# Kernel tuning notes

Hardware: AMD Instinct MI355X
Metric: run time of the kernel (lower is better)

Reference implementation:

```python
import jax, jax.numpy as jnp
import numpy as np


def setup_inputs() -> dict:
    key = jax.random.key(0)
    k1, k2, k3 = jax.random.split(key, 3)
    B, N, L, K, H = 8, 256, 32, 3, 64
    X = jax.random.normal(k1, (B, N, N, L), dtype=jnp.float32)
    G = jax.random.uniform(k2, (K, N, N), dtype=jnp.float32)
    W = jax.random.normal(k3, (K * K * L, H), dtype=jnp.float32) * (2.0 / (K * K * L + H)) ** 0.5
    b = jnp.zeros((H,), dtype=jnp.float32)
    return {"X": X, "G": G, "W": W, "b": b}


def reference(X, G, W, b):
    # X: [b, n, c, l], G: [K, N, N] diffusion supports (n == c == N)
    # Stage 1: diffuse along origin-node axis for all K supports at once.
    m1 = jnp.einsum('bncl,knm->kbmcl', X, G)            # [K, b, m, c, l]
    # Stage 2: diffuse along destination-node axis; lay out so flattening
    # (k, j, l) reproduces torch.cat order (o outer, d inner, feature last).
    m2 = jnp.einsum('kbmcl,jcd->bmdkjl', m1, G)         # [b, m, d, K, K, l]
    B, M, D = m2.shape[0], m2.shape[1], m2.shape[2]
    feat = m2.reshape(B, M, D, -1)                      # [b, m, d, K^2 * l]
    H = jnp.einsum('bmdk,kh->bmdh', feat, W) + b        # [b, m, d, hidden]
    return jax.nn.relu(H)
```

## Files before the change

### kernel.cpp

```cpp
#include <hip/hip_runtime.h>
#include <hip/hip_bf16.h>

#define NB 8
#define NN 256
#define NL 32
#define NQ 8192
#define NH 64
#define SL ((size_t)NQ * NN)

typedef __attribute__((ext_vector_type(8))) short short8v;
typedef __attribute__((ext_vector_type(4))) float float4v;
typedef __attribute__((ext_vector_type(16))) float float16v;

static __device__ __forceinline__ ushort f2bf(float f) {
  __hip_bfloat16 h = __float2bfloat16(f);
  return *reinterpret_cast<const ushort*>(&h);
}
static __device__ __forceinline__ uint packbf(float a, float b) {
  return (uint)f2bf(a) | ((uint)f2bf(b) << 16);
}
static __device__ __forceinline__ void gld_lds16(const void* g, void* l) {
  __builtin_amdgcn_global_load_lds(
      (const __attribute__((address_space(1))) unsigned int*)g,
      (__attribute__((address_space(3))) unsigned int*)l, 16, 0, 0);
}

__global__ __launch_bounds__(256) void prep_g(const float* __restrict__ G,
                                              ushort* __restrict__ Gt) {
  __shared__ float t[32][33];
  const int k = blockIdx.z, m0 = blockIdx.x * 32, n0 = blockIdx.y * 32;
  const int tid = threadIdx.x;
  const int c = tid & 31, r8 = tid >> 5;
#pragma unroll
  for (int i = 0; i < 4; ++i) {
    int r = r8 + i * 8;
    t[r][c] = G[((size_t)k * NN + n0 + r) * NN + m0 + c];
  }
  __syncthreads();
#pragma unroll
  for (int i = 0; i < 4; ++i) {
    int rm = r8 + i * 8;
    Gt[((size_t)k * NN + m0 + rm) * NN + n0 + c] = f2bf(t[c][rm]);
  }
}

__global__ __launch_bounds__(256) void prep_wf(const float* __restrict__ W,
                                               ushort* __restrict__ WtF) {
  const int tid = threadIdx.x;
  for (int e = tid; e < 9 * 2 * 2 * 64; e += 256) {
    const int ln = e & 63, hb = (e >> 6) & 1, kp = (e >> 7) & 1, kj = e >> 8;
    const int h = hb * 32 + (ln & 31);
    const int c0 = kj * 32 + kp * 16 + (ln >> 5) * 8;
    ushort v[8];
#pragma unroll
    for (int i = 0; i < 8; ++i) v[i] = f2bf(W[(size_t)(c0 + i) * NH + h]);
    *(ulong2*)(WtF + (size_t)e * 8) = *(ulong2*)v;
  }
}

__global__ __launch_bounds__(256) void prep_x(const float* __restrict__ X,
                                              ushort* __restrict__ Xt) {
  __shared__ float t[32][33];
  const int qt = blockIdx.x;
  const int n0 = blockIdx.y * 32;
  const int b  = blockIdx.z;
  const int tid = threadIdx.x;
  const int c = tid & 31, r8 = tid >> 5;
  const float* Xb = X + (size_t)b * NN * NQ;
  ushort* Xo = Xt + (size_t)b * SL;
  const size_t q0 = (size_t)qt * 32;
#pragma unroll
  for (int i = 0; i < 4; ++i) {
    int r = r8 + i * 8;
    t[r][c] = Xb[(size_t)(n0 + r) * NQ + q0 + c];
  }
  __syncthreads();
#pragma unroll
  for (int i = 0; i < 4; ++i) {
    int l = r8 + i * 8;
    Xo[((size_t)l * NN + qt) * NN + n0 + c] = f2bf(t[c][l]);
  }
}

__global__ __launch_bounds__(256) void gemm_bt(
    const ushort* __restrict__ A, const ushort* __restrict__ Bt,
    ushort* __restrict__ C, int N, int K,
    size_t aMs, size_t bDs, size_t cs) {
  __shared__ short As[128][40];
  __shared__ short Bs[128][40];
  const int z = blockIdx.z;
  A  += (size_t)(z % 3) * aMs;
  Bt += (size_t)(z / 3) * bDs;
  C  += (size_t)z * cs;
  const int n0 = blockIdx.x * 128;
  const int m0 = blockIdx.y * 128;
  const int tid = threadIdx.x;
  const int lane = tid & 63;
  const int w = tid >> 6;
  const int wr = (w >> 1) * 64, wc = (w & 1) * 64;
  const int sr = tid >> 1, sc = (tid & 1) * 16;
  const int fr = lane & 15, fg = (lane >> 4) * 8;

  float4v acc[4][4] = {};

  const ushort* ap = A + (size_t)(m0 + sr) * K + sc;
  const ushort* bp = Bt + (size_t)(n0 + sr) * K + sc;

  for (int kk = 0; kk < K; kk += 32) {
    *(float4*)&As[sr][sc]     = *(const float4*)(ap + kk);
    *(float4*)&As[sr][sc + 8] = *(const float4*)(ap + kk + 8);
    *(float4*)&Bs[sr][sc]     = *(const float4*)(bp + kk);
    *(float4*)&Bs[sr][sc + 8] = *(const float4*)(bp + kk + 8);
    __syncthreads();
    short8v af[4], bf[4];
#pragma unroll
    for (int i = 0; i < 4; ++i)
      af[i] = *(const short8v*)&As[wr + i * 16 + fr][fg];
#pragma unroll
    for (int j = 0; j < 4; ++j)
      bf[j] = *(const short8v*)&Bs[wc + j * 16 + fr][fg];
#pragma unroll
    for (int i = 0; i < 4; ++i)
#pragma unroll
      for (int j = 0; j < 4; ++j)
        acc[i][j] = __builtin_amdgcn_mfma_f32_16x16x32_bf16(af[i], bf[j],
                                                            acc[i][j], 0, 0, 0);
    __syncthreads();
  }

  const int rbase = (lane >> 4) * 4;
#pragma unroll
  for (int i = 0; i < 4; ++i) {
    const int row = m0 + wr + i * 16 + rbase;
#pragma unroll
    for (int j = 0; j < 4; ++j) {
      const int col = n0 + wc + j * 16 + fr;
      ushort* cp = C + (size_t)row * N + col;
#pragma unroll
      for (int r = 0; r < 4; ++r)
        cp[(size_t)r * N] = f2bf(acc[i][j][r]);
    }
  }
}

__global__ __launch_bounds__(256, 2) void fused_s23(
    const ushort* __restrict__ T1, const ushort* __restrict__ Gt,
    const ushort* __restrict__ WtF, const float* __restrict__ bias,
    float* __restrict__ out) {
  __shared__ ulong2 LDSQ[4096];
  char* base = (char*)LDSQ;

  const int tid = threadIdx.x;
  const int f = blockIdx.x;
  const int lid = (f & 7) * 128 + (f >> 3);
  const int dblk = lid & 1;
  const int mp   = (lid >> 1) & 63;
  const int b    = lid >> 7;

  const int lane = tid & 63;
  const int w  = tid >> 6;
  const int l5 = lane & 31;
  const int h5 = lane >> 5;
  const int wml = (w >> 1) * 64;
  const int wd  = (w & 1) * 64;
  const int d0  = dblk * 128;

  const ushort* t1b  = T1 + ((size_t)b * 3) * SL + (size_t)mp * 128 * 256;
  const ushort* gtb0 = Gt + (size_t)d0 * NN;

  auto stage = [&](int t, int qb) {
    const int kj = t >> 2, q = t & 3;
    const int k = (kj >= 6) ? 2 : (kj >= 3 ? 1 : 0);
    const int j = kj - k * 3;
    const ushort* t1k = t1b + (size_t)k * SL + q * 64;
    const ushort* gtj = gtb0 + (size_t)j * NN * NN + q * 64;
    char* d1 = base + qb + ((tid & 192) << 4);
    char* d2 = d1 + 16384;
#pragma unroll
    for (int i = 0; i < 4; ++i) {
      const int gl = i * 256 + tid;
      const int R  = gl >> 4;
      const int sd = (gl & 15) ^ (R & 15);
      const int dr = 2 * R + (sd >> 3);
      const int g  = sd & 7;
      gld_lds16(t1k + (size_t)dr * 256 + g * 8, d1 + (i << 12));
      gld_lds16(gtj + (size_t)dr * 256 + g * 8, d2 + (i << 12));
    }
  };
  auto ldv = [&](int qb, int toff, int row, int gq) -> short8v {
    const int R = row >> 1;
    const int s = (((row & 1) << 3) + gq) ^ (R & 15);
    return *(const short8v*)(base + qb + toff + (((R << 4) + s) << 4));
  };

  float16v acc3[2][2][2] = {};
  float16v acc2[2][2] = {};

  stage(0, 0);

  for (int t = 0; t < 36; ++t) {
    const int qb = (t & 1) << 15;
    __syncthreads();
    if (t + 1 < 36) stage(t + 1, qb ^ 32768);

#pragma unroll
    for (int ks = 0; ks < 4; ++ks) {
      const int gq = 2 * ks + h5;
      short8v af0 = ldv(qb, 0,     wml + l5,      gq);
      short8v af1 = ldv(qb, 0,     wml + 32 + l5, gq);
      short8v bf0 = ldv(qb, 16384, wd + l5,       gq);
      short8v bf1 = ldv(qb, 16384, wd + 32 + l5,  gq);
      acc2[0][0] = __builtin_amdgcn_mfma_f32_32x32x16_bf16(af0, bf0, acc2[0][0], 0, 0, 0);
      acc2[0][1] = __builtin_amdgcn_mfma_f32_32x32x16_bf16(af0, bf1, acc2[0][1], 0, 0, 0);
      acc2[1][0] = __builtin_amdgcn_mfma_f32_32x32x16_bf16(af1, bf0, acc2[1][0], 0, 0, 0);
      acc2[1][1] = __builtin_amdgcn_mfma_f32_32x32x16_bf16(af1, bf1, acc2[1][1], 0, 0, 0);
    }

    if ((t & 3) == 3) {
      const int kj = t >> 2;
      short8v Af[2][2];
#pragma unroll
      for (int kp = 0; kp < 2; ++kp)
#pragma unroll
        for (int hb = 0; hb < 2; ++hb)
          Af[kp][hb] = *(const short8v*)(WtF +
              ((size_t)(((kj * 2 + kp) * 2 + hb) * 64 + lane)) * 8);

#pragma unroll
      for (int ms = 0; ms < 2; ++ms) {
#pragma unroll
        for (int ds = 0; ds < 2; ++ds) {
          uint P[8], Xc[8];
#pragma unroll
          for (int q = 0; q < 8; ++q)
            P[q] = packbf(acc2[ms][ds][2 * q], acc2[ms][ds][2 * q + 1]);
#pragma unroll
          for (int q = 0; q < 8; ++q) Xc[q] = (uint)__shfl_xor((int)P[q], 32);
          short8v Bf[2];
#pragma unroll
          for (int kp = 0; kp < 2; ++kp) {
            uint4 u;
            if (h5 == 0) {
              u.x = P[4 * kp];      u.y = P[4 * kp + 1];
              u.z = Xc[4 * kp];     u.w = Xc[4 * kp + 1];
            } else {
              u.x = Xc[4 * kp + 2]; u.y = Xc[4 * kp + 3];
              u.z = P[4 * kp + 2];  u.w = P[4 * kp + 3];
            }
            Bf[kp] = *(short8v*)&u;
          }
#pragma unroll
          for (int hb = 0; hb < 2; ++hb) {
#pragma unroll
            for (int kp = 0; kp < 2; ++kp)
              acc3[ms][ds][hb] = __builtin_amdgcn_mfma_f32_32x32x16_bf16(
                  Af[kp][hb], Bf[kp], acc3[ms][ds][hb], 0, 0, 0);
          }
#pragma unroll
          for (int q = 0; q < 16; ++q) acc2[ms][ds][q] = 0.f;
        }
      }
    }
  }

  float4* EP = (float4*)base;
#pragma unroll
  for (int mlp = 0; mlp < 2; ++mlp) {
    __syncthreads();
    if ((w >> 1) == mlp) {
#pragma unroll
      for (int ms = 0; ms < 2; ++ms) {
#pragma unroll
        for (int ds = 0; ds < 2; ++ds) {
          const int d = wd + ds * 32 + l5;
#pragma unroll
          for (int hb = 0; hb < 2; ++hb) {
#pragma unroll
            for (int s = 0; s < 4; ++s) {
              const int hg = 2 * s + h5 + 8 * hb;
              float4 v;
              v.x = acc3[ms][ds][hb][4 * s + 0];
              v.y = acc3[ms][ds][hb][4 * s + 1];
              v.z = acc3[ms][ds][hb][4 * s + 2];
              v.w = acc3[ms][ds][hb][4 * s + 3];
              EP[(ms * 128 + d) * 16 + (hg ^ (d & 15))] = v;
            }
          }
        }
      }
    }
    __syncthreads();
#pragma unroll
    for (int ii = 0; ii < 16; ++ii) {
      const int fi = tid + ii * 256;
      const int ml = fi >> 11;
      const int d  = (fi >> 4) & 127;
      const int hg = fi & 15;
      float4 v = EP[(ml * 128 + d) * 16 + (hg ^ (d & 15))];
      const float4 bb = *(const float4*)(bias + hg * 4);
      v.x = fmaxf(v.x + bb.x, 0.f);
      v.y = fmaxf(v.y + bb.y, 0.f);
      v.z = fmaxf(v.z + bb.z, 0.f);
      v.w = fmaxf(v.w + bb.w, 0.f);
      const int m = mp * 4 + mlp * 2 + ml;
      float* ob = out + (((size_t)b * NN + m) * NN + d0 + d) * NH;
      *(float4*)(ob + hg * 4) = v;
    }
  }
}

extern "C" void kernel_launch(void* const* d_in, const int* in_sizes, int n_in,
                              void* d_out, int out_size, void* d_ws, size_t ws_size,
                              hipStream_t stream) {
  (void)in_sizes; (void)n_in; (void)out_size; (void)ws_size;
  const float* X    = (const float*)d_in[0];
  const float* G    = (const float*)d_in[1];
  const float* W    = (const float*)d_in[2];
  const float* bias = (const float*)d_in[3];
  float* out = (float*)d_out;

  char* p = (char*)d_ws;
  ushort* Gt  = (ushort*)p;  p += (size_t)3 * NN * NN * 2;
  ushort* WtF = (ushort*)p;  p += (size_t)64 * 1024;
  ushort* Xt  = (ushort*)p;  p += (size_t)NB * SL * 2;
  ushort* T1  = (ushort*)p;

  prep_g<<<dim3(8, 8, 3), 256, 0, stream>>>(G, Gt);
  prep_wf<<<dim3(1), 256, 0, stream>>>(W, WtF);
  prep_x<<<dim3(256, 8, NB), 256, 0, stream>>>(X, Xt);

  gemm_bt<<<dim3(NQ / 128, NN / 128, 24), 256, 0, stream>>>(
      Gt, Xt, T1, NQ, NN, (size_t)NN * NN, SL, SL);

  fused_s23<<<dim3(1024), 256, 0, stream>>>(T1, Gt, WtF, bias, out);
}
```

Measured before the change: 209.2 us.

## Rewrite stage-1 GEMM with async LDS double buffering and 32x32 MFMA

```diff
diff --git a/kernel.cpp b/kernel.cpp
--- a/kernel.cpp
+++ b/kernel.cpp
@@ -82,63 +82,83 @@
   }
 }
 
-__global__ __launch_bounds__(256) void gemm_bt(
-    const ushort* __restrict__ A, const ushort* __restrict__ Bt,
-    ushort* __restrict__ C, int N, int K,
-    size_t aMs, size_t bDs, size_t cs) {
-  __shared__ short As[128][40];
-  __shared__ short Bs[128][40];
+__global__ __launch_bounds__(256, 2) void gemm2(
+    const ushort* __restrict__ Gt, const ushort* __restrict__ Xt,
+    ushort* __restrict__ T1) {
+  __shared__ ulong2 LDSQ[4096];
+  char* base = (char*)LDSQ;
+
+  const int tid = threadIdx.x;
   const int z = blockIdx.z;
-  A  += (size_t)(z % 3) * aMs;
-  Bt += (size_t)(z / 3) * bDs;
-  C  += (size_t)z * cs;
-  const int n0 = blockIdx.x * 128;
-  const int m0 = blockIdx.y * 128;
-  const int tid = threadIdx.x;
+  const ushort* Ab = Gt + (size_t)(z % 3) * NN * NN +
+                     (size_t)blockIdx.y * 128 * NN;
+  const ushort* Bb = Xt + (size_t)(z / 3) * SL +
+                     (size_t)blockIdx.x * 128 * NN;
+  ushort* Cb = T1 + (size_t)z * SL;
+
   const int lane = tid & 63;
-  const int w = tid >> 6;
-  const int wr = (w >> 1) * 64, wc = (w & 1) * 64;
-  const int sr = tid >> 1, sc = (tid & 1) * 16;
-  const int fr = lane & 15, fg = (lane >> 4) * 8;
-
-  float4v acc[4][4] = {};
-
-  const ushort* ap = A + (size_t)(m0 + sr) * K + sc;
-  const ushort* bp = Bt + (size_t)(n0 + sr) * K + sc;
-
-  for (int kk = 0; kk < K; kk += 32) {
-    *(float4*)&As[sr][sc]     = *(const float4*)(ap + kk);
-    *(float4*)&As[sr][sc + 8] = *(const float4*)(ap + kk + 8);
-    *(float4*)&Bs[sr][sc]     = *(const float4*)(bp + kk);
-    *(float4*)&Bs[sr][sc + 8] = *(const float4*)(bp + kk + 8);
+  const int w  = tid >> 6;
+  const int l5 = lane & 31;
+  const int h5 = lane >> 5;
+  const int wr = (w >> 1) * 64;
+  const int wc = (w & 1) * 64;
+
+  auto stage = [&](int q, int qb) {
+    const ushort* a = Ab + q * 64;
+    const ushort* bsrc = Bb + q * 64;
+    char* d1 = base + qb + ((tid & 192) << 4);
+    char* d2 = d1 + 16384;
+#pragma unroll
+    for (int i = 0; i < 4; ++i) {
+      const int gl = i * 256 + tid;
+      const int R  = gl >> 4;
+      const int sd = (gl & 15) ^ (R & 15);
+      const int dr = 2 * R + (sd >> 3);
+      const int g  = sd & 7;
+      gld_lds16(a + (size_t)dr * 256 + g * 8, d1 + (i << 12));
+      gld_lds16(bsrc + (size_t)dr * 256 + g * 8, d2 + (i << 12));
+    }
+  };
+  auto ldv = [&](int qb, int toff, int row, int gq) -> short8v {
+    const int R = row >> 1;
+    const int s = (((row & 1) << 3) + gq) ^ (R & 15);
+    return *(const short8v*)(base + qb + toff + (((R << 4) + s) << 4));
+  };
+
+  float16v acc[2][2] = {};
+
+  stage(0, 0);
+
+  for (int q = 0; q < 4; ++q) {
+    const int qb = (q & 1) << 15;
     __syncthreads();
-    short8v af[4], bf[4];
-#pragma unroll
-    for (int i = 0; i < 4; ++i)
-      af[i] = *(const short8v*)&As[wr + i * 16 + fr][fg];
-#pragma unroll
-    for (int j = 0; j < 4; ++j)
-      bf[j] = *(const short8v*)&Bs[wc + j * 16 + fr][fg];
-#pragma unroll
-    for (int i = 0; i < 4; ++i)
-#pragma unroll
-      for (int j = 0; j < 4; ++j)
-        acc[i][j] = __builtin_amdgcn_mfma_f32_16x16x32_bf16(af[i], bf[j],
-                                                            acc[i][j], 0, 0, 0);
-    __syncthreads();
-  }
-
-  const int rbase = (lane >> 4) * 4;
-#pragma unroll
-  for (int i = 0; i < 4; ++i) {
-    const int row = m0 + wr + i * 16 + rbase;
-#pragma unroll
-    for (int j = 0; j < 4; ++j) {
-      const int col = n0 + wc + j * 16 + fr;
-      ushort* cp = C + (size_t)row * N + col;
-#pragma unroll
-      for (int r = 0; r < 4; ++r)
-        cp[(size_t)r * N] = f2bf(acc[i][j][r]);
+    if (q + 1 < 4) stage(q + 1, qb ^ 32768);
+#pragma unroll
+    for (int ks = 0; ks < 4; ++ks) {
+      const int gq = 2 * ks + h5;
+      short8v a0 = ldv(qb, 0,     wr + l5,      gq);
+      short8v a1 = ldv(qb, 0,     wr + 32 + l5, gq);
+      short8v b0 = ldv(qb, 16384, wc + l5,      gq);
+      short8v b1 = ldv(qb, 16384, wc + 32 + l5, gq);
+      acc[0][0] = __builtin_amdgcn_mfma_f32_32x32x16_bf16(a0, b0, acc[0][0], 0, 0, 0);
+      acc[0][1] = __builtin_amdgcn_mfma_f32_32x32x16_bf16(a0, b1, acc[0][1], 0, 0, 0);
+      acc[1][0] = __builtin_amdgcn_mfma_f32_32x32x16_bf16(a1, b0, acc[1][0], 0, 0, 0);
+      acc[1][1] = __builtin_amdgcn_mfma_f32_32x32x16_bf16(a1, b1, acc[1][1], 0, 0, 0);
+    }
+  }
+
+#pragma unroll
+  for (int ms = 0; ms < 2; ++ms) {
+#pragma unroll
+    for (int ds = 0; ds < 2; ++ds) {
+      ushort* cp = Cb +
+          (size_t)(blockIdx.y * 128 + wr + ms * 32 + 4 * h5) * NQ +
+          blockIdx.x * 128 + wc + ds * 32 + l5;
+#pragma unroll
+      for (int r = 0; r < 16; ++r) {
+        const int row = (r & 3) + 8 * (r >> 2);
+        cp[(size_t)row * NQ] = f2bf(acc[ms][ds][r]);
+      }
     }
   }
 }
@@ -329,8 +349,7 @@
   prep_wf<<<dim3(1), 256, 0, stream>>>(W, WtF);
   prep_x<<<dim3(256, 8, NB), 256, 0, stream>>>(X, Xt);
 
-  gemm_bt<<<dim3(NQ / 128, NN / 128, 24), 256, 0, stream>>>(
-      Gt, Xt, T1, NQ, NN, (size_t)NN * NN, SL, SL);
+  gemm2<<<dim3(NQ / 128, NN / 128, 24), 256, 0, stream>>>(Gt, Xt, T1);
 
   fused_s23<<<dim3(1024), 256, 0, stream>>>(T1, Gt, WtF, bias, out);
 }
```

After: 203.8 us. -2.6%, faster.
